# Kernel tuning notes

Measured on AMD Instinct MI355X. Metric: run time of the kernel, lower is better.

Reference implementation:

```python
import jax, jax.numpy as jnp
import numpy as np

N = 10000   # nodes
E = 160000  # edges (avg degree 16)
D_IN = 768
D_HID = 128
HEADS = 4
NEG_SLOPE = 0.2  # PyG GATConv default leaky_relu slope


def setup_inputs() -> dict:
    key = jax.random.key(0)
    ks = jax.random.split(key, 20)
    nrm = lambda k, s, sc: jax.random.normal(k, s, dtype=jnp.float32) * sc
    return {
        "x": nrm(ks[0], (N, D_IN), 1.0),
        "edge_index": jax.random.randint(ks[1], (2, E), 0, N, dtype=jnp.int32),
        "g": nrm(ks[2], (N, D_IN), 1.0),
        # project: Linear(768,128)
        "proj_W": nrm(ks[3], (D_IN, D_HID), D_IN ** -0.5),
        "proj_b": nrm(ks[4], (D_HID,), 0.01),
        # gat1: GATConv(128,128,heads=4), concat -> 512
        "gat1_W": nrm(ks[5], (D_HID, HEADS * D_HID), D_HID ** -0.5),
        "gat1_att_src": nrm(ks[6], (HEADS, D_HID), D_HID ** -0.5),
        "gat1_att_dst": nrm(ks[7], (HEADS, D_HID), D_HID ** -0.5),
        "gat1_bias": nrm(ks[8], (HEADS * D_HID,), 0.01),
        # gat2: GATConv(512,128), heads=1
        "gat2_W": nrm(ks[9], (HEADS * D_HID, D_HID), (HEADS * D_HID) ** -0.5),
        "gat2_att_src": nrm(ks[10], (1, D_HID), D_HID ** -0.5),
        "gat2_att_dst": nrm(ks[11], (1, D_HID), D_HID ** -0.5),
        "gat2_bias": nrm(ks[12], (D_HID,), 0.01),
        # decoder: Linear(128,768)
        "dec_W": nrm(ks[13], (D_HID, D_IN), D_HID ** -0.5),
        "dec_b": nrm(ks[14], (D_IN,), 0.01),
        "beta": jnp.asarray(0.1, dtype=jnp.float32),
    }


def _leaky_relu(x):
    return jnp.where(x > 0, x, NEG_SLOPE * x)


def _gat_conv(x, W, att_src, att_dst, bias, src, dst, n_nodes, heads, out_ch, concat):
    # x: [N, F_in]; edge (src -> dst), aggregation at dst (PyG convention)
    h = (x @ W).reshape(n_nodes, heads, out_ch)            # [N, H, C]
    a_src = jnp.sum(h * att_src, axis=-1)                  # [N, H]
    a_dst = jnp.sum(h * att_dst, axis=-1)                  # [N, H]
    e = _leaky_relu(a_src[src] + a_dst[dst])               # [E, H]
    # segment softmax over incoming edges of each dst node (numerically stable)
    m = jax.lax.stop_gradient(jax.ops.segment_max(e, dst, num_segments=n_nodes))
    ex = jnp.exp(e - m[dst])
    s = jax.ops.segment_sum(ex, dst, num_segments=n_nodes)
    alpha = ex / (s[dst] + 1e-16)                          # [E, H]
    msg = h[src] * alpha[:, :, None]                       # [E, H, C] gather + weight
    out = jax.ops.segment_sum(msg, dst, num_segments=n_nodes)  # scatter-add -> [N, H, C]
    out = out.reshape(n_nodes, heads * out_ch) if concat else out[:, 0, :]
    return out + bias


def reference(x, edge_index, g, proj_W, proj_b,
              gat1_W, gat1_att_src, gat1_att_dst, gat1_bias,
              gat2_W, gat2_att_src, gat2_att_dst, gat2_bias,
              dec_W, dec_b, beta):
    n = x.shape[0]
    # PyG GATConv default add_self_loops=True
    loop = jnp.arange(n, dtype=edge_index.dtype)
    src = jnp.concatenate([edge_index[0], loop])
    dst = jnp.concatenate([edge_index[1], loop])

    xp = x @ proj_W + proj_b                               # [N, 128]
    h = _gat_conv(xp, gat1_W, gat1_att_src, gat1_att_dst, gat1_bias,
                  src, dst, n, HEADS, D_HID, concat=True)  # [N, 512]
    h = jax.nn.elu(h)
    h = _gat_conv(h, gat2_W, gat2_att_src, gat2_att_dst, gat2_bias,
                  src, dst, n, 1, D_HID, concat=False)     # [N, 128]
    gp = g @ proj_W + proj_b                               # [N, 128]
    h = h + beta * gp
    return h @ dec_W + dec_b                               # [N, 768]
```

## Files before the change

### kernel.cpp

```cpp
#include <hip/hip_runtime.h>
#include <math.h>

#define N_NODES 10000
#define N_EDGES 160000
#define ET      (N_EDGES + N_NODES)
#define NRG     313
#define AZS     ((size_t)NRG * 4096)

typedef unsigned short u16;
typedef __attribute__((ext_vector_type(8))) short bf16x8;
typedef __attribute__((ext_vector_type(4))) float f32x4;

__device__ __forceinline__ u16 f2bf(float f) {
    union { float f; unsigned u; } v; v.f = f;
    unsigned r = (v.u + 0x7FFFu + ((v.u >> 16) & 1u)) >> 16;
    return (u16)r;
}
__device__ __forceinline__ float bf2f(u16 b) {
    union { unsigned u; float f; } v; v.u = ((unsigned)b) << 16;
    return v.f;
}

__device__ __forceinline__ void split1(float f, u16& h, u16& l) {
    unsigned u = __float_as_uint(f);
    h = (u16)(u >> 16);
    l = f2bf(f - __uint_as_float(u & 0xffff0000u));
}

__device__ __forceinline__ void splitA8(const float* __restrict__ p,
                                        bf16x8& hv, bf16x8& lv) {
    float4 v0 = *reinterpret_cast<const float4*>(p);
    float4 v1 = *reinterpret_cast<const float4*>(p + 4);
    float f[8] = {v0.x, v0.y, v0.z, v0.w, v1.x, v1.y, v1.z, v1.w};
    bf16x8 h, l;
#pragma unroll
    for (int i = 0; i < 8; ++i) {
        unsigned u = __float_as_uint(f[i]);
        h[i] = (short)(u >> 16);
        float r = f[i] - __uint_as_float(u & 0xffff0000u);
        l[i] = (short)(__float_as_uint(r) >> 16);
    }
    hv = h; lv = l;
}

__device__ __forceinline__ size_t packA_off(int row, int k) {
    int rg = row >> 5, fm = (row >> 4) & 1, lr = row & 15;
    int kb = k >> 5, q = (k >> 3) & 3, j = k & 7;
    return ((((size_t)rg * 4 + kb) * 2 + fm) * 64 + q * 16 + lr) * 8 + j;
}

#define MFMA3(A_h, A_l, B_h, B_l, ACC)                                            \
    ACC = __builtin_amdgcn_mfma_f32_16x16x32_bf16(A_h, B_h, ACC, 0, 0, 0);        \
    ACC = __builtin_amdgcn_mfma_f32_16x16x32_bf16(A_h, B_l, ACC, 0, 0, 0);        \
    ACC = __builtin_amdgcn_mfma_f32_16x16x32_bf16(A_l, B_h, ACC, 0, 0, 0);

#define GLD16(SRC, DST)                                                           \
    __builtin_amdgcn_global_load_lds(                                             \
        (const __attribute__((address_space(1))) void*)(SRC),                     \
        (__attribute__((address_space(3))) void*)(DST), 16, 0, 0)

__global__ void wpack_all_kernel(const float* __restrict__ W0, u16* p0h, u16* p0l,
                                 const float* __restrict__ W1, u16* p1h, u16* p1l,
                                 const float* __restrict__ W2, u16* p2h, u16* p2l,
                                 const float* __restrict__ W3, u16* p3h, u16* p3l) {
    int idx = blockIdx.x * blockDim.x + threadIdx.x;
    const float* W; u16 *oh, *ol; int K, N, rel;
    if      (idx < 12288) { W = W0; oh = p0h; ol = p0l; K = 768; N = 128; rel = idx; }
    else if (idx < 20480) { W = W1; oh = p1h; ol = p1l; K = 128; N = 512; rel = idx - 12288; }
    else if (idx < 28672) { W = W2; oh = p2h; ol = p2l; K = 512; N = 128; rel = idx - 20480; }
    else if (idx < 40960) { W = W3; oh = p3h; ol = p3l; K = 128; N = 768; rel = idx - 28672; }
    else return;
    int perCg = (K / 32) * 128;
    int cg = rel / perCg, r2 = rel - cg * perCg;
    int kb = r2 >> 7, r3 = r2 & 127;
    int fn = r3 >> 6, lane = r3 & 63;
    int col = cg * 32 + fn * 16 + (lane & 15);
    int k0  = kb * 32 + (lane >> 4) * 8;
    bf16x8 hv, lv;
#pragma unroll
    for (int j = 0; j < 8; ++j) {
        float v = W[(size_t)(k0 + j) * N + col];
        u16 h = f2bf(v);
        hv[j] = (short)h;
        lv[j] = (short)f2bf(v - bf2f(h));
    }
    *(bf16x8*)(oh + (size_t)rel * 8) = hv;
    *(bf16x8*)(ol + (size_t)rel * 8) = lv;
}

__global__ void va1_kernel(const float* __restrict__ W1,
                           const float* __restrict__ att_src,
                           const float* __restrict__ att_dst,
                           float* __restrict__ vas, float* __restrict__ vad) {
    int tid = threadIdx.x;
    int k = tid >> 2, h = tid & 3;
    float s = 0.0f, d = 0.0f;
    const float* wr = W1 + (size_t)k * 512 + h * 128;
    const float* as = att_src + h * 128;
    const float* ad = att_dst + h * 128;
    for (int c = 0; c < 128; ++c) {
        float w = wr[c];
        s = fmaf(w, as[c], s);
        d = fmaf(w, ad[c], d);
    }
    vas[k * 4 + h] = s;
    vad[k * 4 + h] = d;
}

template<int K, int SRCSEL, int ZC, int ACT, int LDOUT>
__global__ __launch_bounds__(256)
void mmT_kernel(const float* __restrict__ A0, const float* __restrict__ A1,
                size_t azs,
                const u16* __restrict__ Bh, const u16* __restrict__ Bl,
                const float* __restrict__ bias,
                float* __restrict__ out0, float* __restrict__ out1) {
    constexpr int NS = K / 64;
    __shared__ float smem[2 * 2080];
    const int lane = threadIdx.x & 63;
    const int wid  = threadIdx.x >> 6;
    const int lr = lane & 15, q = lane >> 4;
    const int row0 = blockIdx.x * 32;
    const int z = blockIdx.z;
    const int gcb = blockIdx.y * 128 + z * ZC;

    const float* Ab = SRCSEL ? (z ? A1 : A0) : (A0 + (size_t)z * azs);
    float* outp = (SRCSEL && z) ? out1 : out0;

    const int srow = min(row0 + (lane >> 1), N_NODES - 1);
    const float* sA = Ab + (size_t)srow * K + (lane & 1) * 4;
    float* dg0 = smem + (wid * 2 + 0) * 260;
    float* dg1 = smem + (wid * 2 + 1) * 260;

    const int cg = gcb / 32 + wid;
    const u16* pbh = Bh + (size_t)cg * K * 32 + lane * 8;
    const u16* pbl = Bl + (size_t)cg * K * 32 + lane * 8;

    f32x4 acc[2][2];
#pragma unroll
    for (int i = 0; i < 2; ++i)
#pragma unroll
        for (int j = 0; j < 2; ++j) acc[i][j] = (f32x4){0.f, 0.f, 0.f, 0.f};

    bf16x8 rbh[2][2][2], rbl[2][2][2];

#define STAGE_T(BUF, S) do {                                                   \
        GLD16(sA + (S) * 64 + (wid * 2 + 0) * 8, dg0 + (BUF) * 2080);          \
        GLD16(sA + (S) * 64 + (wid * 2 + 1) * 8, dg1 + (BUF) * 2080);          \
    } while (0)

    STAGE_T(0, 0);
#pragma unroll
    for (int fn = 0; fn < 2; ++fn)
#pragma unroll
        for (int ks = 0; ks < 2; ++ks) {
            rbh[0][fn][ks] = *(const bf16x8*)(pbh + (ks * 2 + fn) * 512);
            rbl[0][fn][ks] = *(const bf16x8*)(pbl + (ks * 2 + fn) * 512);
        }
    __syncthreads();

#pragma unroll
    for (int s = 0; s < NS; ++s) {
        const int bank = s & 1;
        if (s + 1 < NS) {
            STAGE_T(bank ^ 1, s + 1);
#pragma unroll
            for (int fn = 0; fn < 2; ++fn)
#pragma unroll
                for (int ks = 0; ks < 2; ++ks) {
                    rbh[bank ^ 1][fn][ks] =
                        *(const bf16x8*)(pbh + (((s + 1) * 2 + ks) * 2 + fn) * 512);
                    rbl[bank ^ 1][fn][ks] =
                        *(const bf16x8*)(pbl + (((s + 1) * 2 + ks) * 2 + fn) * 512);
                }
        }
        const float* lb = smem + bank * 2080;
        bf16x8 ah[2][2], al[2][2];
#pragma unroll
        for (int fm = 0; fm < 2; ++fm)
#pragma unroll
            for (int ks = 0; ks < 2; ++ks) {
                const float* fp = lb + (ks * 4 + q) * 260 + (fm * 16 + lr) * 8;
                splitA8(fp, ah[fm][ks], al[fm][ks]);
            }
#pragma unroll
        for (int fm = 0; fm < 2; ++fm)
#pragma unroll
            for (int fn = 0; fn < 2; ++fn)
#pragma unroll
                for (int ks = 0; ks < 2; ++ks) {
                    MFMA3(ah[fm][ks], al[fm][ks],
                          rbh[bank][fn][ks], rbl[bank][fn][ks], acc[fm][fn]);
                }
        __syncthreads();
    }

    int orq = q * 4;
#pragma unroll
    for (int fm = 0; fm < 2; ++fm)
#pragma unroll
        for (int fn = 0; fn < 2; ++fn) {
            int col = gcb + wid * 32 + fn * 16 + lr;
            float bb = bias ? bias[col] : 0.0f;
#pragma unroll
            for (int i = 0; i < 4; ++i) {
                int orow = row0 + fm * 16 + orq + i;
                if (orow < N_NODES) {
                    float r = acc[fm][fn][i] + bb;
                    if (ACT == 1) r = r > 0.0f ? r : expm1f(r);
                    outp[(size_t)orow * LDOUT + col] = r;
                }
            }
        }
#undef STAGE_T
}

template<int ZC, int ACT, int LDOUT>
__global__ __launch_bounds__(256)
void mmP_kernel(const u16* __restrict__ Ah, const u16* __restrict__ Al,
                size_t azs,
                const u16* __restrict__ Bh, const u16* __restrict__ Bl,
                const float* __restrict__ bias,
                float* __restrict__ out) {
    constexpr int K = 128;
    const int lane = threadIdx.x & 63;
    const int wid  = threadIdx.x >> 6;
    const int lr = lane & 15, q = lane >> 4;
    const int rg = blockIdx.x;
    const int row0 = rg * 32;
    const int z = blockIdx.z;
    const int gcb = blockIdx.y * 128 + z * ZC;

    const u16* ah = Ah + (size_t)z * azs + (size_t)rg * 4096 + lane * 8;
    const u16* al = Al + (size_t)z * azs + (size_t)rg * 4096 + lane * 8;
    const int cg = gcb / 32 + wid;
    const u16* bh = Bh + (size_t)cg * K * 32 + lane * 8;
    const u16* bl = Bl + (size_t)cg * K * 32 + lane * 8;

    f32x4 acc[2][2];
#pragma unroll
    for (int i = 0; i < 2; ++i)
#pragma unroll
        for (int j = 0; j < 2; ++j) acc[i][j] = (f32x4){0.f, 0.f, 0.f, 0.f};

#pragma unroll
    for (int kb = 0; kb < 4; ++kb) {
        bf16x8 a0h = *(const bf16x8*)(ah + (kb * 2 + 0) * 512);
        bf16x8 a1h = *(const bf16x8*)(ah + (kb * 2 + 1) * 512);
        bf16x8 a0l = *(const bf16x8*)(al + (kb * 2 + 0) * 512);
        bf16x8 a1l = *(const bf16x8*)(al + (kb * 2 + 1) * 512);
        bf16x8 b0h = *(const bf16x8*)(bh + (kb * 2 + 0) * 512);
        bf16x8 b1h = *(const bf16x8*)(bh + (kb * 2 + 1) * 512);
        bf16x8 b0l = *(const bf16x8*)(bl + (kb * 2 + 0) * 512);
        bf16x8 b1l = *(const bf16x8*)(bl + (kb * 2 + 1) * 512);
        MFMA3(a0h, a0l, b0h, b0l, acc[0][0]);
        MFMA3(a0h, a0l, b1h, b1l, acc[0][1]);
        MFMA3(a1h, a1l, b0h, b0l, acc[1][0]);
        MFMA3(a1h, a1l, b1h, b1l, acc[1][1]);
    }

    int orq = q * 4;
#pragma unroll
    for (int fm = 0; fm < 2; ++fm)
#pragma unroll
        for (int fn = 0; fn < 2; ++fn) {
            int col = gcb + wid * 32 + fn * 16 + lr;
            float bb = bias[col];
#pragma unroll
            for (int i = 0; i < 4; ++i) {
                int orow = row0 + fm * 16 + orq + i;
                if (orow < N_NODES) {
                    float r = acc[fm][fn][i] + bb;
                    if (ACT == 1) r = r > 0.0f ? r : expm1f(r);
                    out[(size_t)orow * LDOUT + col] = r;
                }
            }
        }
}

__global__ void att1_kernel(const float* __restrict__ xp,
                            const float* __restrict__ vas,
                            const float* __restrict__ vad,
                            float* __restrict__ as, float* __restrict__ ad) {
    int wv = threadIdx.x >> 6, lane = threadIdx.x & 63;
    int n = blockIdx.x * 4 + wv;
    float2 v = *reinterpret_cast<const float2*>(xp + (size_t)n * 128 + lane * 2);
    float4 s0 = *reinterpret_cast<const float4*>(vas + (lane * 2) * 4);
    float4 s1 = *reinterpret_cast<const float4*>(vas + (lane * 2 + 1) * 4);
    float4 d0 = *reinterpret_cast<const float4*>(vad + (lane * 2) * 4);
    float4 d1 = *reinterpret_cast<const float4*>(vad + (lane * 2 + 1) * 4);
    float ss[4] = { v.x * s0.x + v.y * s1.x, v.x * s0.y + v.y * s1.y,
                    v.x * s0.z + v.y * s1.z, v.x * s0.w + v.y * s1.w };
    float dd[4] = { v.x * d0.x + v.y * d1.x, v.x * d0.y + v.y * d1.y,
                    v.x * d0.z + v.y * d1.z, v.x * d0.w + v.y * d1.w };
#pragma unroll
    for (int m = 32; m > 0; m >>= 1)
#pragma unroll
        for (int h = 0; h < 4; ++h) {
            ss[h] += __shfl_xor(ss[h], m, 64);
            dd[h] += __shfl_xor(dd[h], m, 64);
        }
    if (lane == 0) {
#pragma unroll
        for (int h = 0; h < 4; ++h) {
            as[(size_t)n * 4 + h] = ss[h];
            ad[(size_t)n * 4 + h] = dd[h];
        }
    }
}

__global__ void att2_kernel(const float* __restrict__ h,
                            const float* __restrict__ att_src,
                            const float* __restrict__ att_dst,
                            float* __restrict__ as, float* __restrict__ ad) {
    int wv = threadIdx.x >> 6, lane = threadIdx.x & 63;
    int n = blockIdx.x * 4 + wv;
    const float* hp = h + (size_t)n * 128 + lane * 2;
    float2 v = *reinterpret_cast<const float2*>(hp);
    float2 a = *reinterpret_cast<const float2*>(att_src + lane * 2);
    float2 b = *reinterpret_cast<const float2*>(att_dst + lane * 2);
    float ss = v.x * a.x + v.y * a.y;
    float sd = v.x * b.x + v.y * b.y;
#pragma unroll
    for (int m = 32; m > 0; m >>= 1) {
        ss += __shfl_xor(ss, m, 64);
        sd += __shfl_xor(sd, m, 64);
    }
    if (lane == 0) { as[n] = ss; ad[n] = sd; }
}

__global__ void zero_int_kernel(int* __restrict__ p, int n) {
    int i = blockIdx.x * blockDim.x + threadIdx.x;
    if (i < n) p[i] = 0;
}

__global__ void deg_kernel(const int* __restrict__ ei, int* __restrict__ deg) {
    int e = blockIdx.x * blockDim.x + threadIdx.x;
    if (e >= ET) return;
    int d = (e < N_EDGES) ? ei[N_EDGES + e] : (e - N_EDGES);
    atomicAdd(&deg[d], 1);
}

__global__ void scan1_kernel(const int* __restrict__ deg, int* __restrict__ bsum) {
    __shared__ int sm[256];
    int i = blockIdx.x * 256 + threadIdx.x;
    sm[threadIdx.x] = (i < N_NODES) ? deg[i] : 0;
    __syncthreads();
    for (int s = 128; s > 0; s >>= 1) {
        if (threadIdx.x < s) sm[threadIdx.x] += sm[threadIdx.x + s];
        __syncthreads();
    }
    if (threadIdx.x == 0) bsum[blockIdx.x] = sm[0];
}

__global__ void scan2_kernel(const int* __restrict__ bsum, int* __restrict__ boff,
                             int* __restrict__ off) {
    int lane = threadIdx.x;
    int v = (lane < 40) ? bsum[lane] : 0;
    int inc = v;
#pragma unroll
    for (int s = 1; s < 64; s <<= 1) {
        int t = __shfl_up(inc, s, 64);
        if (lane >= s) inc += t;
    }
    if (lane < 40) boff[lane] = inc - v;
    if (lane == 63) off[N_NODES] = inc;
}

__global__ void scan3_kernel(const int* __restrict__ deg, const int* __restrict__ boff,
                             int* __restrict__ off, int* __restrict__ cur) {
    __shared__ int sm[256];
    int i = blockIdx.x * 256 + threadIdx.x;
    int v = (i < N_NODES) ? deg[i] : 0;
    sm[threadIdx.x] = v;
    __syncthreads();
    for (int s = 1; s < 256; s <<= 1) {
        int t = (threadIdx.x >= s) ? sm[threadIdx.x - s] : 0;
        __syncthreads();
        sm[threadIdx.x] += t;
        __syncthreads();
    }
    if (i < N_NODES) {
        int ex = boff[blockIdx.x] + sm[threadIdx.x] - v;
        off[i] = ex;
        cur[i] = ex;
    }
}

__global__ void fill_kernel(const int* __restrict__ ei,
                            int* __restrict__ cur, int* __restrict__ csr_src) {
    int e = blockIdx.x * blockDim.x + threadIdx.x;
    if (e >= ET) return;
    int s, d;
    if (e < N_EDGES) { s = ei[e]; d = ei[N_EDGES + e]; }
    else             { s = e - N_EDGES; d = s; }
    int pos = atomicAdd(&cur[d], 1);
    csr_src[pos] = s;
}

template<int H>
__global__ void softmax_kernel(const float* __restrict__ as,
                               const float* __restrict__ ad,
                               const int* __restrict__ off,
                               const int* __restrict__ csr_src,
                               float* __restrict__ exw,
                               float* __restrict__ inv_s) {
    int wv = threadIdx.x >> 6, lane = threadIdx.x & 63;
    int n = blockIdx.x * 4 + wv;
    int o0 = off[n], o1 = off[n + 1];
    float adn[H], m[H], s[H];
#pragma unroll
    for (int h = 0; h < H; ++h) { adn[h] = ad[(size_t)n * H + h]; m[h] = -1e30f; s[h] = 0.0f; }

    for (int j = o0 + lane; j < o1; j += 64) {
        int sn = csr_src[j];
#pragma unroll
        for (int h = 0; h < H; ++h) {
            float e = as[(size_t)sn * H + h] + adn[h];
            e = e > 0.0f ? e : 0.2f * e;
            m[h] = fmaxf(m[h], e);
        }
    }
#pragma unroll
    for (int mk = 32; mk > 0; mk >>= 1)
#pragma unroll
        for (int h = 0; h < H; ++h) m[h] = fmaxf(m[h], __shfl_xor(m[h], mk, 64));

    for (int j = o0 + lane; j < o1; j += 64) {
        int sn = csr_src[j];
        float exv[H];
#pragma unroll
        for (int h = 0; h < H; ++h) {
            float e = as[(size_t)sn * H + h] + adn[h];
            e = e > 0.0f ? e : 0.2f * e;
            exv[h] = expf(e - m[h]);
            s[h] += exv[h];
        }
        if (H == 4) {
            *reinterpret_cast<float4*>(exw + (size_t)j * 4) =
                make_float4(exv[0], exv[1], exv[2 % H], exv[3 % H]);
        } else {
            exw[j] = exv[0];
        }
    }
#pragma unroll
    for (int mk = 32; mk > 0; mk >>= 1)
#pragma unroll
        for (int h = 0; h < H; ++h) s[h] += __shfl_xor(s[h], mk, 64);

    if (lane == 0) {
#pragma unroll
        for (int h = 0; h < H; ++h) inv_s[(size_t)n * H + h] = 1.0f / (s[h] + 1e-16f);
    }
}

__global__ void agg1_kernel(const float* __restrict__ xp,
                            const float* __restrict__ exw,
                            const float* __restrict__ inv_s,
                            const int* __restrict__ off,
                            const int* __restrict__ csr_src,
                            u16* __restrict__ aggPh, u16* __restrict__ aggPl) {
    int sub = threadIdx.x >> 7;
    int c   = threadIdx.x & 127;
    int n   = blockIdx.x * 2 + sub;
    int o0 = off[n], o1 = off[n + 1];

    float a0 = 0.f, a1 = 0.f, a2 = 0.f, a3 = 0.f;
    int j = o0;
    for (; j + 2 <= o1; j += 2) {
        int s0 = csr_src[j], s1 = csr_src[j + 1];
        float4 w0 = *reinterpret_cast<const float4*>(exw + (size_t)j * 4);
        float4 w1 = *reinterpret_cast<const float4*>(exw + (size_t)(j + 1) * 4);
        float v0 = xp[(size_t)s0 * 128 + c];
        float v1 = xp[(size_t)s1 * 128 + c];
        a0 = fmaf(w0.x, v0, a0); a1 = fmaf(w0.y, v0, a1);
        a2 = fmaf(w0.z, v0, a2); a3 = fmaf(w0.w, v0, a3);
        a0 = fmaf(w1.x, v1, a0); a1 = fmaf(w1.y, v1, a1);
        a2 = fmaf(w1.z, v1, a2); a3 = fmaf(w1.w, v1, a3);
    }
    if (j < o1) {
        int s0 = csr_src[j];
        float4 w0 = *reinterpret_cast<const float4*>(exw + (size_t)j * 4);
        float v0 = xp[(size_t)s0 * 128 + c];
        a0 = fmaf(w0.x, v0, a0); a1 = fmaf(w0.y, v0, a1);
        a2 = fmaf(w0.z, v0, a2); a3 = fmaf(w0.w, v0, a3);
    }

    float4 inv = *reinterpret_cast<const float4*>(inv_s + (size_t)n * 4);
    float r[4] = {a0 * inv.x, a1 * inv.y, a2 * inv.z, a3 * inv.w};
    size_t po = packA_off(n, c);
#pragma unroll
    for (int h = 0; h < 4; ++h) {
        u16 hi, lo;
        split1(r[h], hi, lo);
        aggPh[(size_t)h * AZS + po] = hi;
        aggPl[(size_t)h * AZS + po] = lo;
    }
}

template<int NPB>
__global__ void gather2_kernel(const float* __restrict__ h,
                               const float* __restrict__ exw,
                               const float* __restrict__ inv_s,
                               const int* __restrict__ off,
                               const int* __restrict__ csr_src,
                               const float* __restrict__ bias,
                               u16* __restrict__ outPh, u16* __restrict__ outPl,
                               const float* __restrict__ gp,
                               const float* __restrict__ beta_p) {
    int sub = threadIdx.x >> 7;
    int c   = threadIdx.x & 127;
    int n   = blockIdx.x * NPB + sub;
    int o0 = off[n], o1 = off[n + 1];

    float acc = 0.0f;
    int j = o0;
    for (; j + 4 <= o1; j += 4) {
        int s0 = csr_src[j + 0], s1 = csr_src[j + 1];
        int s2 = csr_src[j + 2], s3 = csr_src[j + 3];
        float w0 = exw[j + 0], w1 = exw[j + 1];
        float w2 = exw[j + 2], w3 = exw[j + 3];
        float v0 = h[(size_t)s0 * 128 + c];
        float v1 = h[(size_t)s1 * 128 + c];
        float v2 = h[(size_t)s2 * 128 + c];
        float v3 = h[(size_t)s3 * 128 + c];
        acc = fmaf(w0, v0, acc);
        acc = fmaf(w1, v1, acc);
        acc = fmaf(w2, v2, acc);
        acc = fmaf(w3, v3, acc);
    }
    for (; j < o1; ++j) {
        acc = fmaf(exw[j], h[(size_t)csr_src[j] * 128 + c], acc);
    }

    float r = acc * inv_s[n] + bias[c] + beta_p[0] * gp[(size_t)n * 128 + c];
    u16 hi, lo;
    split1(r, hi, lo);
    size_t po = packA_off(n, c);
    outPh[po] = hi;
    outPl[po] = lo;
}

extern "C" void kernel_launch(void* const* d_in, const int* in_sizes, int n_in,
                              void* d_out, int out_size, void* d_ws, size_t ws_size,
                              hipStream_t stream) {
    const float* x      = (const float*)d_in[0];
    const int*   ei     = (const int*)  d_in[1];
    const float* g      = (const float*)d_in[2];
    const float* proj_W = (const float*)d_in[3];
    const float* proj_b = (const float*)d_in[4];
    const float* gat1_W = (const float*)d_in[5];
    const float* g1_as  = (const float*)d_in[6];
    const float* g1_ad  = (const float*)d_in[7];
    const float* gat1_b = (const float*)d_in[8];
    const float* gat2_W = (const float*)d_in[9];
    const float* g2_as  = (const float*)d_in[10];
    const float* g2_ad  = (const float*)d_in[11];
    const float* gat2_b = (const float*)d_in[12];
    const float* dec_W  = (const float*)d_in[13];
    const float* dec_b  = (const float*)d_in[14];
    const float* beta   = (const float*)d_in[15];
    float* out = (float*)d_out;

    char* p = (char*)d_ws;
    auto alloc = [&](size_t b) { void* r = (void*)p; p += (b + 255) & ~(size_t)255; return r; };
    float* helu  = (float*)alloc((size_t)10000 * 512 * 4);
    u16*   aggPh = (u16*)alloc(4 * AZS * 2);
    u16*   aggPl = (u16*)alloc(4 * AZS * 2);
    u16*   hfPh  = (u16*)alloc(AZS * 2);
    u16*   hfPl  = (u16*)alloc(AZS * 2);
    float* xp    = (float*)alloc((size_t)10000 * 128 * 4);
    float* gp    = (float*)alloc((size_t)10000 * 128 * 4);
    u16*   pwh   = (u16*)alloc(768 * 128 * 2);
    u16*   pwl   = (u16*)alloc(768 * 128 * 2);
    u16*   w1h   = (u16*)alloc(128 * 512 * 2);
    u16*   w1l   = (u16*)alloc(128 * 512 * 2);
    u16*   w2h   = (u16*)alloc(512 * 128 * 2);
    u16*   w2l   = (u16*)alloc(512 * 128 * 2);
    u16*   wdh   = (u16*)alloc(128 * 768 * 2);
    u16*   wdl   = (u16*)alloc(128 * 768 * 2);
    float* va1s  = (float*)alloc(128 * 4 * 4);
    float* va1d  = (float*)alloc(128 * 4 * 4);
    float* a1s   = (float*)alloc((size_t)N_NODES * 4 * 4);
    float* a1d   = (float*)alloc((size_t)N_NODES * 4 * 4);
    float* a2s   = (float*)alloc((size_t)N_NODES * 4);
    float* a2d   = (float*)alloc((size_t)N_NODES * 4);
    float* is1   = (float*)alloc((size_t)N_NODES * 4 * 4);
    float* is2   = (float*)alloc((size_t)N_NODES * 4);
    float* exw4  = (float*)alloc((size_t)ET * 4 * 4);
    float* exw1  = (float*)alloc((size_t)ET * 4);
    int*   deg   = (int*)alloc((size_t)N_NODES * 4);
    int*   off   = (int*)alloc((size_t)(N_NODES + 1) * 4);
    int*   cur   = (int*)alloc((size_t)N_NODES * 4);
    int*   csr   = (int*)alloc((size_t)ET * 4);
    int*   bsum  = (int*)alloc(64 * 4);
    int*   boff  = (int*)alloc(64 * 4);
    float* h2 = xp;

    hipLaunchKernelGGL(wpack_all_kernel, dim3(160), dim3(256), 0, stream,
                       proj_W, pwh, pwl, gat1_W, w1h, w1l,
                       gat2_W, w2h, w2l, dec_W, wdh, wdl);
    hipLaunchKernelGGL(va1_kernel, dim3(1), dim3(512), 0, stream,
                       gat1_W, g1_as, g1_ad, va1s, va1d);
    hipLaunchKernelGGL(zero_int_kernel, dim3((N_NODES + 255) / 256), dim3(256), 0, stream, deg, N_NODES);
    hipLaunchKernelGGL(deg_kernel, dim3((ET + 255) / 256), dim3(256), 0, stream, ei, deg);
    hipLaunchKernelGGL(scan1_kernel, dim3(40), dim3(256), 0, stream, deg, bsum);
    hipLaunchKernelGGL(scan2_kernel, dim3(1), dim3(64), 0, stream, bsum, boff, off);
    hipLaunchKernelGGL(scan3_kernel, dim3(40), dim3(256), 0, stream, deg, boff, off, cur);
    hipLaunchKernelGGL(fill_kernel, dim3((ET + 255) / 256), dim3(256), 0, stream, ei, cur, csr);

    hipLaunchKernelGGL((mmT_kernel<768, 1, 0, 0, 128>), dim3(NRG, 1, 2), dim3(256), 0, stream,
                       x, g, (size_t)0, pwh, pwl, proj_b, xp, gp);

    hipLaunchKernelGGL(att1_kernel, dim3(N_NODES / 4), dim3(256), 0, stream,
                       xp, va1s, va1d, a1s, a1d);
    hipLaunchKernelGGL(softmax_kernel<4>, dim3(N_NODES / 4), dim3(256), 0, stream,
                       a1s, a1d, off, csr, exw4, is1);
    hipLaunchKernelGGL(agg1_kernel, dim3(N_NODES / 2), dim3(256), 0, stream,
                       xp, exw4, is1, off, csr, aggPh, aggPl);
    hipLaunchKernelGGL((mmP_kernel<128, 1, 512>), dim3(NRG, 1, 4), dim3(256), 0, stream,
                       aggPh, aggPl, AZS, w1h, w1l, gat1_b, helu);

    hipLaunchKernelGGL((mmT_kernel<512, 0, 0, 0, 128>), dim3(NRG, 1, 1), dim3(256), 0, stream,
                       helu, (const float*)nullptr, (size_t)0,
                       w2h, w2l, (const float*)nullptr, h2, (float*)nullptr);
    hipLaunchKernelGGL(att2_kernel, dim3(N_NODES / 4), dim3(256), 0, stream,
                       h2, g2_as, g2_ad, a2s, a2d);
    hipLaunchKernelGGL(softmax_kernel<1>, dim3(N_NODES / 4), dim3(256), 0, stream,
                       a2s, a2d, off, csr, exw1, is2);
    hipLaunchKernelGGL((gather2_kernel<2>), dim3(N_NODES / 2), dim3(256), 0, stream,
                       h2, exw1, is2, off, csr, gat2_b, hfPh, hfPl, gp, beta);

    hipLaunchKernelGGL((mmP_kernel<0, 0, 768>), dim3(NRG, 6, 1), dim3(256), 0, stream,
                       hfPh, hfPl, (size_t)0, wdh, wdl, dec_b, out);
}
```

Baseline: 201.3 us.

## Fuse segment softmax into aggregation kernels and merge prep/scan launches

Folds the per-destination softmax into the gather-aggregate kernels for both GAT layers. Each block now computes the max, the sum and the per-edge exponentials on the fly, staging edge weights and source indices in shared memory, so the exw and inv_s buffers are never written or read from global memory. Weight packing, attention-vector precompute and degree zeroing are merged into one prep kernel, and the small scan2 kernel is folded into scan3, which cuts the launch count. The cost is that edge scores are recomputed three times per edge, and blocks are one node of 128 threads with several syncthreads, which may lower occupancy and latency hiding.

```diff
diff --git a/kernel.cpp b/kernel.cpp
--- a/kernel.cpp
+++ b/kernel.cpp
@@ -59,52 +59,57 @@
         (const __attribute__((address_space(1))) void*)(SRC),                     \
         (__attribute__((address_space(3))) void*)(DST), 16, 0, 0)
 
-__global__ void wpack_all_kernel(const float* __restrict__ W0, u16* p0h, u16* p0l,
-                                 const float* __restrict__ W1, u16* p1h, u16* p1l,
-                                 const float* __restrict__ W2, u16* p2h, u16* p2l,
-                                 const float* __restrict__ W3, u16* p3h, u16* p3l) {
-    int idx = blockIdx.x * blockDim.x + threadIdx.x;
-    const float* W; u16 *oh, *ol; int K, N, rel;
-    if      (idx < 12288) { W = W0; oh = p0h; ol = p0l; K = 768; N = 128; rel = idx; }
-    else if (idx < 20480) { W = W1; oh = p1h; ol = p1l; K = 128; N = 512; rel = idx - 12288; }
-    else if (idx < 28672) { W = W2; oh = p2h; ol = p2l; K = 512; N = 128; rel = idx - 20480; }
-    else if (idx < 40960) { W = W3; oh = p3h; ol = p3l; K = 128; N = 768; rel = idx - 28672; }
-    else return;
-    int perCg = (K / 32) * 128;
-    int cg = rel / perCg, r2 = rel - cg * perCg;
-    int kb = r2 >> 7, r3 = r2 & 127;
-    int fn = r3 >> 6, lane = r3 & 63;
-    int col = cg * 32 + fn * 16 + (lane & 15);
-    int k0  = kb * 32 + (lane >> 4) * 8;
-    bf16x8 hv, lv;
-#pragma unroll
-    for (int j = 0; j < 8; ++j) {
-        float v = W[(size_t)(k0 + j) * N + col];
-        u16 h = f2bf(v);
-        hv[j] = (short)h;
-        lv[j] = (short)f2bf(v - bf2f(h));
-    }
-    *(bf16x8*)(oh + (size_t)rel * 8) = hv;
-    *(bf16x8*)(ol + (size_t)rel * 8) = lv;
-}
-
-__global__ void va1_kernel(const float* __restrict__ W1,
-                           const float* __restrict__ att_src,
-                           const float* __restrict__ att_dst,
-                           float* __restrict__ vas, float* __restrict__ vad) {
-    int tid = threadIdx.x;
-    int k = tid >> 2, h = tid & 3;
-    float s = 0.0f, d = 0.0f;
-    const float* wr = W1 + (size_t)k * 512 + h * 128;
-    const float* as = att_src + h * 128;
-    const float* ad = att_dst + h * 128;
-    for (int c = 0; c < 128; ++c) {
-        float w = wr[c];
-        s = fmaf(w, as[c], s);
-        d = fmaf(w, ad[c], d);
-    }
-    vas[k * 4 + h] = s;
-    vad[k * 4 + h] = d;
+__global__ void prep_kernel(const float* __restrict__ W0, u16* p0h, u16* p0l,
+                            const float* __restrict__ W1, u16* p1h, u16* p1l,
+                            const float* __restrict__ W2, u16* p2h, u16* p2l,
+                            const float* __restrict__ W3, u16* p3h, u16* p3l,
+                            const float* __restrict__ att_src,
+                            const float* __restrict__ att_dst,
+                            float* __restrict__ vas, float* __restrict__ vad,
+                            int* __restrict__ deg) {
+    int b = blockIdx.x, tid = threadIdx.x;
+    if (b < 160) {
+        int idx = b * 256 + tid;
+        const float* W; u16 *oh, *ol; int K, N, rel;
+        if      (idx < 12288) { W = W0; oh = p0h; ol = p0l; K = 768; N = 128; rel = idx; }
+        else if (idx < 20480) { W = W1; oh = p1h; ol = p1l; K = 128; N = 512; rel = idx - 12288; }
+        else if (idx < 28672) { W = W2; oh = p2h; ol = p2l; K = 512; N = 128; rel = idx - 20480; }
+        else                  { W = W3; oh = p3h; ol = p3l; K = 128; N = 768; rel = idx - 28672; }
+        int perCg = (K / 32) * 128;
+        int cg = rel / perCg, r2 = rel - cg * perCg;
+        int kb = r2 >> 7, r3 = r2 & 127;
+        int fn = r3 >> 6, lane = r3 & 63;
+        int col = cg * 32 + fn * 16 + (lane & 15);
+        int k0  = kb * 32 + (lane >> 4) * 8;
+        bf16x8 hv, lv;
+#pragma unroll
+        for (int j = 0; j < 8; ++j) {
+            float v = W[(size_t)(k0 + j) * N + col];
+            u16 h = f2bf(v);
+            hv[j] = (short)h;
+            lv[j] = (short)f2bf(v - bf2f(h));
+        }
+        *(bf16x8*)(oh + (size_t)rel * 8) = hv;
+        *(bf16x8*)(ol + (size_t)rel * 8) = lv;
+    } else if (b == 160) {
+        for (int it = tid; it < 512; it += 256) {
+            int k = it >> 2, h = it & 3;
+            float s = 0.0f, d = 0.0f;
+            const float* wr = W1 + (size_t)k * 512 + h * 128;
+            const float* as = att_src + h * 128;
+            const float* ad = att_dst + h * 128;
+            for (int c = 0; c < 128; ++c) {
+                float w = wr[c];
+                s = fmaf(w, as[c], s);
+                d = fmaf(w, ad[c], d);
+            }
+            vas[k * 4 + h] = s;
+            vad[k * 4 + h] = d;
+        }
+    } else {
+        int i = (b - 161) * 256 + tid;
+        if (i < N_NODES) deg[i] = 0;
+    }
 }
 
 template<int K, int SRCSEL, int ZC, int ACT, int LDOUT>
@@ -328,11 +333,6 @@
     if (lane == 0) { as[n] = ss; ad[n] = sd; }
 }
 
-__global__ void zero_int_kernel(int* __restrict__ p, int n) {
-    int i = blockIdx.x * blockDim.x + threadIdx.x;
-    if (i < n) p[i] = 0;
-}
-
 __global__ void deg_kernel(const int* __restrict__ ei, int* __restrict__ deg) {
     int e = blockIdx.x * blockDim.x + threadIdx.x;
     if (e >= ET) return;
@@ -352,38 +352,34 @@
     if (threadIdx.x == 0) bsum[blockIdx.x] = sm[0];
 }
 
-__global__ void scan2_kernel(const int* __restrict__ bsum, int* __restrict__ boff,
-                             int* __restrict__ off) {
-    int lane = threadIdx.x;
-    int v = (lane < 40) ? bsum[lane] : 0;
-    int inc = v;
-#pragma unroll
-    for (int s = 1; s < 64; s <<= 1) {
-        int t = __shfl_up(inc, s, 64);
-        if (lane >= s) inc += t;
-    }
-    if (lane < 40) boff[lane] = inc - v;
-    if (lane == 63) off[N_NODES] = inc;
-}
-
-__global__ void scan3_kernel(const int* __restrict__ deg, const int* __restrict__ boff,
+__global__ void scan3_kernel(const int* __restrict__ deg, const int* __restrict__ bsum,
                              int* __restrict__ off, int* __restrict__ cur) {
     __shared__ int sm[256];
-    int i = blockIdx.x * 256 + threadIdx.x;
+    __shared__ int sb[40];
+    __shared__ int bofs;
+    int tid = threadIdx.x;
+    if (tid < 40) sb[tid] = bsum[tid];
+    int i = blockIdx.x * 256 + tid;
     int v = (i < N_NODES) ? deg[i] : 0;
-    sm[threadIdx.x] = v;
+    sm[tid] = v;
     __syncthreads();
+    if (tid == 0) {
+        int s = 0;
+        for (int b = 0; b < blockIdx.x; ++b) s += sb[b];
+        bofs = s;
+    }
     for (int s = 1; s < 256; s <<= 1) {
-        int t = (threadIdx.x >= s) ? sm[threadIdx.x - s] : 0;
-        __syncthreads();
-        sm[threadIdx.x] += t;
+        int t = (tid >= s) ? sm[tid - s] : 0;
+        __syncthreads();
+        sm[tid] += t;
         __syncthreads();
     }
     if (i < N_NODES) {
-        int ex = boff[blockIdx.x] + sm[threadIdx.x] - v;
+        int ex = bofs + sm[tid] - v;
         off[i] = ex;
         cur[i] = ex;
     }
+    if (blockIdx.x == 0 && tid == 0) off[N_NODES] = ET;
 }
 
 __global__ void fill_kernel(const int* __restrict__ ei,
@@ -397,97 +393,87 @@
     csr_src[pos] = s;
 }
 
-template<int H>
-__global__ void softmax_kernel(const float* __restrict__ as,
-                               const float* __restrict__ ad,
-                               const int* __restrict__ off,
-                               const int* __restrict__ csr_src,
-                               float* __restrict__ exw,
-                               float* __restrict__ inv_s) {
-    int wv = threadIdx.x >> 6, lane = threadIdx.x & 63;
-    int n = blockIdx.x * 4 + wv;
+__global__ __launch_bounds__(128)
+void smagg1_kernel(const float* __restrict__ xp,
+                   const float* __restrict__ a1s, const float* __restrict__ a1d,
+                   const int* __restrict__ off, const int* __restrict__ csr,
+                   u16* __restrict__ aggPh, u16* __restrict__ aggPl) {
+    int n = blockIdx.x;
+    int tid = threadIdx.x, lane = tid & 63, wv = tid >> 6;
     int o0 = off[n], o1 = off[n + 1];
-    float adn[H], m[H], s[H];
-#pragma unroll
-    for (int h = 0; h < H; ++h) { adn[h] = ad[(size_t)n * H + h]; m[h] = -1e30f; s[h] = 0.0f; }
-
-    for (int j = o0 + lane; j < o1; j += 64) {
-        int sn = csr_src[j];
-#pragma unroll
-        for (int h = 0; h < H; ++h) {
-            float e = as[(size_t)sn * H + h] + adn[h];
-            e = e > 0.0f ? e : 0.2f * e;
-            m[h] = fmaxf(m[h], e);
-        }
+    __shared__ float red[2][8];
+    __shared__ float wsh[128][4];
+    __shared__ int   ssh[128];
+
+    float4 adv = *reinterpret_cast<const float4*>(a1d + (size_t)n * 4);
+    float adn[4] = {adv.x, adv.y, adv.z, adv.w};
+
+    float m[4] = {-1e30f, -1e30f, -1e30f, -1e30f};
+    for (int j = o0 + tid; j < o1; j += 128) {
+        int sn = csr[j];
+        float4 asv = *reinterpret_cast<const float4*>(a1s + (size_t)sn * 4);
+        float e0 = asv.x + adn[0]; e0 = e0 > 0.f ? e0 : 0.2f * e0; m[0] = fmaxf(m[0], e0);
+        float e1 = asv.y + adn[1]; e1 = e1 > 0.f ? e1 : 0.2f * e1; m[1] = fmaxf(m[1], e1);
+        float e2 = asv.z + adn[2]; e2 = e2 > 0.f ? e2 : 0.2f * e2; m[2] = fmaxf(m[2], e2);
+        float e3 = asv.w + adn[3]; e3 = e3 > 0.f ? e3 : 0.2f * e3; m[3] = fmaxf(m[3], e3);
     }
 #pragma unroll
     for (int mk = 32; mk > 0; mk >>= 1)
 #pragma unroll
-        for (int h = 0; h < H; ++h) m[h] = fmaxf(m[h], __shfl_xor(m[h], mk, 64));
-
-    for (int j = o0 + lane; j < o1; j += 64) {
-        int sn = csr_src[j];
-        float exv[H];
-#pragma unroll
-        for (int h = 0; h < H; ++h) {
-            float e = as[(size_t)sn * H + h] + adn[h];
-            e = e > 0.0f ? e : 0.2f * e;
-            exv[h] = expf(e - m[h]);
-            s[h] += exv[h];
-        }
-        if (H == 4) {
-            *reinterpret_cast<float4*>(exw + (size_t)j * 4) =
-                make_float4(exv[0], exv[1], exv[2 % H], exv[3 % H]);
-        } else {
-            exw[j] = exv[0];
-        }
+        for (int h = 0; h < 4; ++h) m[h] = fmaxf(m[h], __shfl_xor(m[h], mk, 64));
+    if (lane == 0)
+#pragma unroll
+        for (int h = 0; h < 4; ++h) red[wv][h] = m[h];
+    __syncthreads();
+#pragma unroll
+    for (int h = 0; h < 4; ++h) m[h] = fmaxf(red[0][h], red[1][h]);
+
+    float s4[4] = {0.f, 0.f, 0.f, 0.f};
+    for (int j = o0 + tid; j < o1; j += 128) {
+        int sn = csr[j];
+        float4 asv = *reinterpret_cast<const float4*>(a1s + (size_t)sn * 4);
+        float e0 = asv.x + adn[0]; e0 = e0 > 0.f ? e0 : 0.2f * e0; s4[0] += expf(e0 - m[0]);
+        float e1 = asv.y + adn[1]; e1 = e1 > 0.f ? e1 : 0.2f * e1; s4[1] += expf(e1 - m[1]);
+        float e2 = asv.z + adn[2]; e2 = e2 > 0.f ? e2 : 0.2f * e2; s4[2] += expf(e2 - m[2]);
+        float e3 = asv.w + adn[3]; e3 = e3 > 0.f ? e3 : 0.2f * e3; s4[3] += expf(e3 - m[3]);
     }
 #pragma unroll
     for (int mk = 32; mk > 0; mk >>= 1)
 #pragma unroll
-        for (int h = 0; h < H; ++h) s[h] += __shfl_xor(s[h], mk, 64);
-
-    if (lane == 0) {
-#pragma unroll
-        for (int h = 0; h < H; ++h) inv_s[(size_t)n * H + h] = 1.0f / (s[h] + 1e-16f);
-    }
-}
-
-__global__ void agg1_kernel(const float* __restrict__ xp,
-                            const float* __restrict__ exw,
-                            const float* __restrict__ inv_s,
-                            const int* __restrict__ off,
-                            const int* __restrict__ csr_src,
-                            u16* __restrict__ aggPh, u16* __restrict__ aggPl) {
-    int sub = threadIdx.x >> 7;
-    int c   = threadIdx.x & 127;
-    int n   = blockIdx.x * 2 + sub;
-    int o0 = off[n], o1 = off[n + 1];
+        for (int h = 0; h < 4; ++h) s4[h] += __shfl_xor(s4[h], mk, 64);
+    if (lane == 0)
+#pragma unroll
+        for (int h = 0; h < 4; ++h) red[wv][4 + h] = s4[h];
+    __syncthreads();
+    float inv[4];
+#pragma unroll
+    for (int h = 0; h < 4; ++h) inv[h] = 1.0f / (red[0][4 + h] + red[1][4 + h] + 1e-16f);
 
     float a0 = 0.f, a1 = 0.f, a2 = 0.f, a3 = 0.f;
-    int j = o0;
-    for (; j + 2 <= o1; j += 2) {
-        int s0 = csr_src[j], s1 = csr_src[j + 1];
-        float4 w0 = *reinterpret_cast<const float4*>(exw + (size_t)j * 4);
-        float4 w1 = *reinterpret_cast<const float4*>(exw + (size_t)(j + 1) * 4);
-        float v0 = xp[(size_t)s0 * 128 + c];
-        float v1 = xp[(size_t)s1 * 128 + c];
-        a0 = fmaf(w0.x, v0, a0); a1 = fmaf(w0.y, v0, a1);
-        a2 = fmaf(w0.z, v0, a2); a3 = fmaf(w0.w, v0, a3);
-        a0 = fmaf(w1.x, v1, a0); a1 = fmaf(w1.y, v1, a1);
-        a2 = fmaf(w1.z, v1, a2); a3 = fmaf(w1.w, v1, a3);
-    }
-    if (j < o1) {
-        int s0 = csr_src[j];
-        float4 w0 = *reinterpret_cast<const float4*>(exw + (size_t)j * 4);
-        float v0 = xp[(size_t)s0 * 128 + c];
-        a0 = fmaf(w0.x, v0, a0); a1 = fmaf(w0.y, v0, a1);
-        a2 = fmaf(w0.z, v0, a2); a3 = fmaf(w0.w, v0, a3);
-    }
-
-    float4 inv = *reinterpret_cast<const float4*>(inv_s + (size_t)n * 4);
-    float r[4] = {a0 * inv.x, a1 * inv.y, a2 * inv.z, a3 * inv.w};
-    size_t po = packA_off(n, c);
+    for (int base = o0; base < o1; base += 128) {
+        __syncthreads();
+        int j = base + tid;
+        if (j < o1) {
+            int sn = csr[j];
+            ssh[tid] = sn;
+            float4 asv = *reinterpret_cast<const float4*>(a1s + (size_t)sn * 4);
+            float e0 = asv.x + adn[0]; e0 = e0 > 0.f ? e0 : 0.2f * e0; wsh[tid][0] = expf(e0 - m[0]);
+            float e1 = asv.y + adn[1]; e1 = e1 > 0.f ? e1 : 0.2f * e1; wsh[tid][1] = expf(e1 - m[1]);
+            float e2 = asv.z + adn[2]; e2 = e2 > 0.f ? e2 : 0.2f * e2; wsh[tid][2] = expf(e2 - m[2]);
+            float e3 = asv.w + adn[3]; e3 = e3 > 0.f ? e3 : 0.2f * e3; wsh[tid][3] = expf(e3 - m[3]);
+        }
+        __syncthreads();
+        int cnt = min(128, o1 - base);
+        for (int e2i = 0; e2i < cnt; ++e2i) {
+            float v = xp[(size_t)ssh[e2i] * 128 + tid];
+            float4 w = *reinterpret_cast<const float4*>(&wsh[e2i][0]);
+            a0 = fmaf(w.x, v, a0); a1 = fmaf(w.y, v, a1);
+            a2 = fmaf(w.z, v, a2); a3 = fmaf(w.w, v, a3);
+        }
+    }
+
+    float r[4] = {a0 * inv[0], a1 * inv[1], a2 * inv[2], a3 * inv[3]};
+    size_t po = packA_off(n, tid);
 #pragma unroll
     for (int h = 0; h < 4; ++h) {
         u16 hi, lo;
@@ -497,45 +483,68 @@
     }
 }
 
-template<int NPB>
-__global__ void gather2_kernel(const float* __restrict__ h,
-                               const float* __restrict__ exw,
-                               const float* __restrict__ inv_s,
-                               const int* __restrict__ off,
-                               const int* __restrict__ csr_src,
-                               const float* __restrict__ bias,
-                               u16* __restrict__ outPh, u16* __restrict__ outPl,
-                               const float* __restrict__ gp,
-                               const float* __restrict__ beta_p) {
-    int sub = threadIdx.x >> 7;
-    int c   = threadIdx.x & 127;
-    int n   = blockIdx.x * NPB + sub;
+__global__ __launch_bounds__(128)
+void smgather2_kernel(const float* __restrict__ h2,
+                      const float* __restrict__ a2s, const float* __restrict__ a2d,
+                      const int* __restrict__ off, const int* __restrict__ csr,
+                      const float* __restrict__ bias,
+                      u16* __restrict__ outPh, u16* __restrict__ outPl,
+                      const float* __restrict__ gp,
+                      const float* __restrict__ beta_p) {
+    int n = blockIdx.x;
+    int tid = threadIdx.x, lane = tid & 63, wv = tid >> 6;
     int o0 = off[n], o1 = off[n + 1];
-
-    float acc = 0.0f;
-    int j = o0;
-    for (; j + 4 <= o1; j += 4) {
-        int s0 = csr_src[j + 0], s1 = csr_src[j + 1];
-        int s2 = csr_src[j + 2], s3 = csr_src[j + 3];
-        float w0 = exw[j + 0], w1 = exw[j + 1];
-        float w2 = exw[j + 2], w3 = exw[j + 3];
-        float v0 = h[(size_t)s0 * 128 + c];
-        float v1 = h[(size_t)s1 * 128 + c];
-        float v2 = h[(size_t)s2 * 128 + c];
-        float v3 = h[(size_t)s3 * 128 + c];
-        acc = fmaf(w0, v0, acc);
-        acc = fmaf(w1, v1, acc);
-        acc = fmaf(w2, v2, acc);
-        acc = fmaf(w3, v3, acc);
-    }
-    for (; j < o1; ++j) {
-        acc = fmaf(exw[j], h[(size_t)csr_src[j] * 128 + c], acc);
-    }
-
-    float r = acc * inv_s[n] + bias[c] + beta_p[0] * gp[(size_t)n * 128 + c];
+    __shared__ float red[2][2];
+    __shared__ float wsh[128];
+    __shared__ int   ssh[128];
+
+    float adn = a2d[n];
+    float m = -1e30f;
+    for (int j = o0 + tid; j < o1; j += 128) {
+        float e = a2s[csr[j]] + adn;
+        e = e > 0.f ? e : 0.2f * e;
+        m = fmaxf(m, e);
+    }
+#pragma unroll
+    for (int mk = 32; mk > 0; mk >>= 1) m = fmaxf(m, __shfl_xor(m, mk, 64));
+    if (lane == 0) red[wv][0] = m;
+    __syncthreads();
+    m = fmaxf(red[0][0], red[1][0]);
+
+    float s = 0.f;
+    for (int j = o0 + tid; j < o1; j += 128) {
+        float e = a2s[csr[j]] + adn;
+        e = e > 0.f ? e : 0.2f * e;
+        s += expf(e - m);
+    }
+#pragma unroll
+    for (int mk = 32; mk > 0; mk >>= 1) s += __shfl_xor(s, mk, 64);
+    if (lane == 0) red[wv][1] = s;
+    __syncthreads();
+    float inv = 1.0f / (red[0][1] + red[1][1] + 1e-16f);
+
+    float acc = 0.f;
+    for (int base = o0; base < o1; base += 128) {
+        __syncthreads();
+        int j = base + tid;
+        if (j < o1) {
+            int sn = csr[j];
+            ssh[tid] = sn;
+            float e = a2s[sn] + adn;
+            e = e > 0.f ? e : 0.2f * e;
+            wsh[tid] = expf(e - m);
+        }
+        __syncthreads();
+        int cnt = min(128, o1 - base);
+        for (int e2i = 0; e2i < cnt; ++e2i) {
+            acc = fmaf(wsh[e2i], h2[(size_t)ssh[e2i] * 128 + tid], acc);
+        }
+    }
+
+    float r = acc * inv + bias[tid] + beta_p[0] * gp[(size_t)n * 128 + tid];
     u16 hi, lo;
     split1(r, hi, lo);
-    size_t po = packA_off(n, c);
+    size_t po = packA_off(n, tid);
     outPh[po] = hi;
     outPl[po] = lo;
 }
@@ -584,28 +593,20 @@
     float* a1d   = (float*)alloc((size_t)N_NODES * 4 * 4);
     float* a2s   = (float*)alloc((size_t)N_NODES * 4);
     float* a2d   = (float*)alloc((size_t)N_NODES * 4);
-    float* is1   = (float*)alloc((size_t)N_NODES * 4 * 4);
-    float* is2   = (float*)alloc((size_t)N_NODES * 4);
-    float* exw4  = (float*)alloc((size_t)ET * 4 * 4);
-    float* exw1  = (float*)alloc((size_t)ET * 4);
     int*   deg   = (int*)alloc((size_t)N_NODES * 4);
     int*   off   = (int*)alloc((size_t)(N_NODES + 1) * 4);
     int*   cur   = (int*)alloc((size_t)N_NODES * 4);
     int*   csr   = (int*)alloc((size_t)ET * 4);
     int*   bsum  = (int*)alloc(64 * 4);
-    int*   boff  = (int*)alloc(64 * 4);
     float* h2 = xp;
 
-    hipLaunchKernelGGL(wpack_all_kernel, dim3(160), dim3(256), 0, stream,
+    hipLaunchKernelGGL(prep_kernel, dim3(201), dim3(256), 0, stream,
                        proj_W, pwh, pwl, gat1_W, w1h, w1l,
-                       gat2_W, w2h, w2l, dec_W, wdh, wdl);
-    hipLaunchKernelGGL(va1_kernel, dim3(1), dim3(512), 0, stream,
-                       gat1_W, g1_as, g1_ad, va1s, va1d);
-    hipLaunchKernelGGL(zero_int_kernel, dim3((N_NODES + 255) / 256), dim3(256), 0, stream, deg, N_NODES);
+                       gat2_W, w2h, w2l, dec_W, wdh, wdl,
+                       g1_as, g1_ad, va1s, va1d, deg);
     hipLaunchKernelGGL(deg_kernel, dim3((ET + 255) / 256), dim3(256), 0, stream, ei, deg);
     hipLaunchKernelGGL(scan1_kernel, dim3(40), dim3(256), 0, stream, deg, bsum);
-    hipLaunchKernelGGL(scan2_kernel, dim3(1), dim3(64), 0, stream, bsum, boff, off);
-    hipLaunchKernelGGL(scan3_kernel, dim3(40), dim3(256), 0, stream, deg, boff, off, cur);
+    hipLaunchKernelGGL(scan3_kernel, dim3(40), dim3(256), 0, stream, deg, bsum, off, cur);
     hipLaunchKernelGGL(fill_kernel, dim3((ET + 255) / 256), dim3(256), 0, stream, ei, cur, csr);
 
     hipLaunchKernelGGL((mmT_kernel<768, 1, 0, 0, 128>), dim3(NRG, 1, 2), dim3(256), 0, stream,
@@ -613,10 +614,8 @@
 
     hipLaunchKernelGGL(att1_kernel, dim3(N_NODES / 4), dim3(256), 0, stream,
                        xp, va1s, va1d, a1s, a1d);
-    hipLaunchKernelGGL(softmax_kernel<4>, dim3(N_NODES / 4), dim3(256), 0, stream,
-                       a1s, a1d, off, csr, exw4, is1);
-    hipLaunchKernelGGL(agg1_kernel, dim3(N_NODES / 2), dim3(256), 0, stream,
-                       xp, exw4, is1, off, csr, aggPh, aggPl);
+    hipLaunchKernelGGL(smagg1_kernel, dim3(N_NODES), dim3(128), 0, stream,
+                       xp, a1s, a1d, off, csr, aggPh, aggPl);
     hipLaunchKernelGGL((mmP_kernel<128, 1, 512>), dim3(NRG, 1, 4), dim3(256), 0, stream,
                        aggPh, aggPl, AZS, w1h, w1l, gat1_b, helu);
 
@@ -625,10 +624,8 @@
                        w2h, w2l, (const float*)nullptr, h2, (float*)nullptr);
     hipLaunchKernelGGL(att2_kernel, dim3(N_NODES / 4), dim3(256), 0, stream,
                        h2, g2_as, g2_ad, a2s, a2d);
-    hipLaunchKernelGGL(softmax_kernel<1>, dim3(N_NODES / 4), dim3(256), 0, stream,
-                       a2s, a2d, off, csr, exw1, is2);
-    hipLaunchKernelGGL((gather2_kernel<2>), dim3(N_NODES / 2), dim3(256), 0, stream,
-                       h2, exw1, is2, off, csr, gat2_b, hfPh, hfPl, gp, beta);
+    hipLaunchKernelGGL(smgather2_kernel, dim3(N_NODES), dim3(128), 0, stream,
+                       h2, a2s, a2d, off, csr, gat2_b, hfPh, hfPl, gp, beta);
 
     hipLaunchKernelGGL((mmP_kernel<0, 0, 768>), dim3(NRG, 6, 1), dim3(256), 0, stream,
                        hfPh, hfPl, (size_t)0, wdh, wdl, dec_b, out);
```

Result: faster. 180.0 us (median of 2 runs) (-10.6%).
